# Kernel tuning notes

Measured on AMD Instinct MI355X. Metric: run time of the kernel, lower is better.

The kernel has to match this reference:

```python
import jax, jax.numpy as jnp
import numpy as np

V, T, E, H, B, S = 50000, 45, 256, 512, 32, 256


def setup_inputs() -> dict:
    key = jax.random.key(0)
    ks = jax.random.split(key, 14)
    s = 0.05
    return dict(
        x=jax.random.randint(ks[0], (B, S), 0, V),
        tags=jax.random.randint(ks[1], (B, S), 0, T),
        mask=jnp.ones((B, S), dtype=bool),
        emb=jax.random.normal(ks[2], (V, E), jnp.float32),
        Wih_f=jax.random.normal(ks[3], (4 * H, E), jnp.float32) * s,
        Whh_f=jax.random.normal(ks[4], (4 * H, H), jnp.float32) * s,
        bih_f=jnp.zeros((4 * H,), jnp.float32),
        bhh_f=jnp.zeros((4 * H,), jnp.float32),
        Wih_b=jax.random.normal(ks[5], (4 * H, E), jnp.float32) * s,
        Whh_b=jax.random.normal(ks[6], (4 * H, H), jnp.float32) * s,
        bih_b=jnp.zeros((4 * H,), jnp.float32),
        bhh_b=jnp.zeros((4 * H,), jnp.float32),
        Wout=jax.random.normal(ks[7], (T, 2 * H), jnp.float32) * s,
        bout=jnp.zeros((T,), jnp.float32),
        start=jax.random.normal(ks[8], (T,), jnp.float32) * 0.1,
        end=jax.random.normal(ks[9], (T,), jnp.float32) * 0.1,
        trans=jax.random.normal(ks[10], (T, T), jnp.float32) * 0.1,
    )


def _lstm_dir(xp, Whh, reverse):
    # xp: [S, B, 4H] precomputed input projection + biases; gate order i,f,g,o (torch)
    Bn = xp.shape[1]
    Hn = Whh.shape[1]
    def step(carry, g_in):
        h, c = carry
        g = g_in + h @ Whh.T
        i, f, gg, o = jnp.split(g, 4, axis=-1)
        c = jax.nn.sigmoid(f) * c + jax.nn.sigmoid(i) * jnp.tanh(gg)
        h = jax.nn.sigmoid(o) * jnp.tanh(c)
        return (h, c), h
    init = (jnp.zeros((Bn, Hn), xp.dtype), jnp.zeros((Bn, Hn), xp.dtype))
    _, hs = jax.lax.scan(step, init, xp, reverse=reverse)
    return hs  # [S, B, H]


def _crf_nll(emissions, tags, mask, start, end, trans):
    # emissions: [B, S, T]; neg mean log-likelihood (torchcrf, reduction='mean')
    mf = mask.astype(emissions.dtype)
    em_tag = jnp.take_along_axis(emissions, tags[:, :, None], axis=2)[:, :, 0]  # [B,S]
    num = start[tags[:, 0]] + em_tag[:, 0]
    num = num + ((trans[tags[:, :-1], tags[:, 1:]] + em_tag[:, 1:]) * mf[:, 1:]).sum(1)
    seq_ends = mf.sum(1).astype(tags.dtype) - 1
    last_tags = jnp.take_along_axis(tags, seq_ends[:, None], axis=1)[:, 0]
    num = num + end[last_tags]
    def denom_step(alpha, inp):
        em_t, m_t = inp  # [B,T], [B]
        nxt = jax.nn.logsumexp(alpha[:, :, None] + trans[None, :, :] + em_t[:, None, :], axis=1)
        return jnp.where(m_t[:, None] > 0, nxt, alpha), None
    alpha0 = start[None, :] + emissions[:, 0]
    em_rest = emissions.transpose(1, 0, 2)[1:]  # [S-1, B, T]
    alpha, _ = jax.lax.scan(denom_step, alpha0, (em_rest, mf.T[1:]))
    logZ = jax.nn.logsumexp(alpha + end[None, :], axis=1)
    return -(num - logZ).mean()


def reference(x, tags, mask, emb, Wih_f, Whh_f, bih_f, bhh_f,
              Wih_b, Whh_b, bih_b, bhh_b, Wout, bout, start, end, trans):
    embeds = emb[x]                      # [B, S, E]
    xs = embeds.transpose(1, 0, 2)       # [S, B, E]
    xp_f = jnp.einsum('sbe,ge->sbg', xs, Wih_f) + bih_f + bhh_f
    hs_f = _lstm_dir(xp_f, Whh_f, False)
    xp_b = jnp.einsum('sbe,ge->sbg', xs, Wih_b) + bih_b + bhh_b
    hs_b = _lstm_dir(xp_b, Whh_b, True)
    hcat = jnp.concatenate([hs_f, hs_b], axis=-1)          # [S, B, 2H]
    emissions = jnp.einsum('sbh,th->sbt', hcat, Wout) + bout
    emissions = emissions.transpose(1, 0, 2)                # [B, S, T]
    return _crf_nll(emissions, tags, mask, start, end, trans)
```

## Files before the change

kernel.cpp:

```cpp
#include <hip/hip_runtime.h>
#include <stdint.h>

#define S_LEN 256
#define B_N 32
#define H_N 512
#define E_N 256
#define T_N 45
#define G4H 2048

typedef unsigned short u16;
typedef unsigned int u32;
typedef u16 u16x8 __attribute__((ext_vector_type(8)));
typedef u16 u16x4 __attribute__((ext_vector_type(4)));
typedef u32 u32x4 __attribute__((ext_vector_type(4)));
typedef __bf16 bf16x8 __attribute__((ext_vector_type(8)));
typedef float f32x4 __attribute__((ext_vector_type(4)));
typedef unsigned long long u64;

#define OFF_FLG   0ull
#define OFF_ATOK  1024ull
#define OFF_WIHF  (OFF_ATOK + 4194304ull)
#define OFF_WIHB  (OFF_WIHF + 1048576ull)
#define OFF_WHHF  (OFF_WIHB + 1048576ull)
#define OFF_WHHB  (OFF_WHHF + 2097152ull)
#define OFF_WOUT  (OFF_WHHB + 2097152ull)
#define OFF_BSF   (OFF_WOUT + 98304ull)
#define OFF_BSB   (OFF_BSF + 8192ull)
#define OFF_XPF   (OFF_BSB + 8192ull)
#define OFF_XPB   (OFF_XPF + 33554432ull)
#define OFF_HSF   (OFF_XPB + 33554432ull)
#define OFF_HSB   (OFF_HSF + 8421376ull)
#define OFF_EM    (OFF_HSB + 8421376ull)
#define OFF_VAL   (OFF_EM + 1572864ull)

__device__ __forceinline__ u16 f2bf(float f) {
  union { float f; unsigned u; } v; v.f = f;
  unsigned r = v.u + 0x7FFFu + ((v.u >> 16) & 1u);
  return (u16)(r >> 16);
}
__device__ __forceinline__ float bf2f(u16 b) {
  union { unsigned u; float f; } v; v.u = ((unsigned)b) << 16;
  return v.f;
}
__device__ __forceinline__ bf16x8 ld8(const u16* p) {
  u16x8 v = *reinterpret_cast<const u16x8*>(p);
  return __builtin_bit_cast(bf16x8, v);
}
__device__ __forceinline__ void st_h8cc(u16* p, u16x4 v) {
  __hip_atomic_store(reinterpret_cast<u64*>(p), __builtin_bit_cast(u64, v),
                     __ATOMIC_RELAXED, __HIP_MEMORY_SCOPE_AGENT);
}
__device__ __forceinline__ u32x4 ld16cc(const u16* p) {
  u32x4 r;
  asm volatile("global_load_dwordx4 %0, %1, off sc0 sc1"
               : "=v"(r) : "v"(p) : "memory");
  return r;
}
__device__ __forceinline__ f32x4 mfma16(bf16x8 a, bf16x8 b, f32x4 c) {
  return __builtin_amdgcn_mfma_f32_16x16x32_bf16(a, b, c, 0, 0, 0);
}
__device__ __forceinline__ float sigm(float x) { return 1.f / (1.f + __expf(-x)); }
__device__ __forceinline__ float tanhf_(float x) {
  float ax = fabsf(x);
  float e = __expf(-2.f * ax);
  float t = 1.f - 2.f * e / (1.f + e);
  return (x < 0.f) ? -t : t;
}
__device__ __forceinline__ float wredmax(float v) {
  #pragma unroll
  for (int m = 1; m < 64; m <<= 1) v = fmaxf(v, __shfl_xor(v, m));
  return v;
}
__device__ __forceinline__ float wredsum(float v) {
  #pragma unroll
  for (int m = 1; m < 64; m <<= 1) v += __shfl_xor(v, m);
  return v;
}

__global__ void k_castA(const int* __restrict__ x, const float* __restrict__ emb,
                        u16* __restrict__ atok) {
  int idx = blockIdx.x * 256 + threadIdx.x;
  int t = idx >> 5;
  int e0 = (idx & 31) << 3;
  int s = t >> 5, b = t & 31;
  int xid = x[b * S_LEN + s];
  const float4* p = reinterpret_cast<const float4*>(emb + (size_t)xid * E_N + e0);
  float4 lo = p[0], hi = p[1];
  u16x8 o;
  o[0] = f2bf(lo.x); o[1] = f2bf(lo.y); o[2] = f2bf(lo.z); o[3] = f2bf(lo.w);
  o[4] = f2bf(hi.x); o[5] = f2bf(hi.y); o[6] = f2bf(hi.z); o[7] = f2bf(hi.w);
  *reinterpret_cast<u16x8*>(atok + (size_t)t * E_N + e0) = o;
}

__global__ void k_castW(const float* __restrict__ WihF, const float* __restrict__ WihB,
                        const float* __restrict__ WhhF, const float* __restrict__ WhhB,
                        const float* __restrict__ Wout,
                        const float* __restrict__ bihF, const float* __restrict__ bhhF,
                        const float* __restrict__ bihB, const float* __restrict__ bhhB,
                        u16* wihf, u16* wihb, u16* whhf, u16* whhb, u16* woutp,
                        float* bsf, float* bsb, u16* hsf, u16* hsb) {
  int i = blockIdx.x * 256 + threadIdx.x;
  if (i < 524288) { wihf[i] = f2bf(WihF[i]); return; }
  i -= 524288;
  if (i < 524288) { wihb[i] = f2bf(WihB[i]); return; }
  i -= 524288;
  if (i < 1048576) { whhf[i] = f2bf(WhhF[i]); return; }
  i -= 1048576;
  if (i < 1048576) { whhb[i] = f2bf(WhhB[i]); return; }
  i -= 1048576;
  if (i < 49152) {
    int n = i >> 10, k = i & 1023;
    woutp[i] = (n < T_N) ? f2bf(Wout[n * 1024 + k]) : (u16)0;
    return;
  }
  i -= 49152;
  if (i < 2048) { bsf[i] = bihF[i] + bhhF[i]; return; }
  i -= 2048;
  if (i < 2048) { bsb[i] = bihB[i] + bhhB[i]; return; }
  i -= 2048;
  if (i < 16384) { hsf[i] = 0; return; }
  i -= 16384;
  if (i < 16384) { hsb[(size_t)256 * 16384 + i] = 0; return; }
}

__global__ __launch_bounds__(256) void k_gemm_xp(
    const u16* __restrict__ atok, const u16* __restrict__ wihF, const u16* __restrict__ wihB,
    const float* __restrict__ bsF, const float* __restrict__ bsB,
    u16* __restrict__ xpF, u16* __restrict__ xpB) {
  int wid = blockIdx.x;
  int dir = wid >> 10, rem = wid & 1023;
  const int wave = threadIdx.x >> 6, lane = threadIdx.x & 63;
  const int lr = lane & 15, lh = lane >> 4;
  const int t0 = (rem >> 3) * 64;
  const int g0 = (rem & 7) * 256 + wave * 64;
  const u16* wih = dir ? wihB : wihF;
  const float* bs = dir ? bsB : bsF;
  u16* xp = dir ? xpB : xpF;
  f32x4 acc[4][4] = {};
  for (int kk = 0; kk < 8; ++kk) {
    int e = kk * 32 + lh * 8;
    bf16x8 a[4], bfr[4];
    #pragma unroll
    for (int mi = 0; mi < 4; ++mi) a[mi] = ld8(atok + (size_t)(t0 + 16 * mi + lr) * E_N + e);
    #pragma unroll
    for (int ni = 0; ni < 4; ++ni) bfr[ni] = ld8(wih + (size_t)(g0 + 16 * ni + lr) * E_N + e);
    #pragma unroll
    for (int mi = 0; mi < 4; ++mi)
      #pragma unroll
      for (int ni = 0; ni < 4; ++ni) acc[mi][ni] = mfma16(a[mi], bfr[ni], acc[mi][ni]);
  }
  #pragma unroll
  for (int ni = 0; ni < 4; ++ni) {
    int g = g0 + 16 * ni + lr;
    float bsv = bs[g];
    #pragma unroll
    for (int mi = 0; mi < 4; ++mi)
      #pragma unroll
      for (int r = 0; r < 4; ++r) {
        int t = t0 + 16 * mi + 4 * lh + r;
        xp[(size_t)t * G4H + g] = f2bf(acc[mi][ni][r] + bsv);
      }
  }
}

__global__ __launch_bounds__(128, 1) void k_lstm(
    const u16* __restrict__ whhF, const u16* __restrict__ whhB,
    const u16* __restrict__ xpF, const u16* __restrict__ xpB,
    u16* __restrict__ hsF, u16* __restrict__ hsB, int* flags) {
  const int dir = blockIdx.x >> 5;
  const int w = blockIdx.x & 31;
  const int nt = threadIdx.x >> 6;
  const int lane = threadIdx.x & 63;
  const int lr = lane & 15, lh = lane >> 4;
  const u16* whh = dir ? whhB : whhF;
  const u16* xp = dir ? xpB : xpF;
  u16* hs = dir ? hsB : hsF;
  int* flg = flags + dir * 64;
  const int myf = w * 2 + nt;

  bf16x8 A[4][16];
  #pragma unroll
  for (int mt = 0; mt < 4; ++mt) {
    const u16* base = whh + (size_t)(mt * 512 + 16 * w + lr) * H_N + lh * 8;
    #pragma unroll
    for (int kk = 0; kk < 16; ++kk) A[mt][kk] = ld8(base + kk * 32);
  }
  const int b = nt * 16 + lr;
  const int j0 = 16 * w + 4 * lh;
  float cst[4] = {0.f, 0.f, 0.f, 0.f};

  for (int t = 0; t < S_LEN; ++t) {
    const int s = dir ? (S_LEN - 1 - t) : t;
    const int slot_r = dir ? (s + 1) : s;
    const int slot_w = dir ? s : (s + 1);
    u16x4 xq[4];
    const u16* xpt = xp + ((size_t)(s * B_N + b)) * G4H + j0;
    #pragma unroll
    for (int mt = 0; mt < 4; ++mt) xq[mt] = *reinterpret_cast<const u16x4*>(xpt + mt * 512);

    if (t > 0) {
      for (;;) {
        int f = __hip_atomic_load(&flg[lane], __ATOMIC_RELAXED, __HIP_MEMORY_SCOPE_AGENT);
        if (__all(f >= t)) break;
        __builtin_amdgcn_s_sleep(1);
      }
    }

    const u16* hp = hs + ((size_t)slot_r * B_N + b) * H_N + lh * 8;
    u32x4 raw[16];
    #pragma unroll
    for (int kk = 0; kk < 16; ++kk) raw[kk] = ld16cc(hp + kk * 32);
    asm volatile("s_waitcnt vmcnt(0)" ::: "memory");
    __builtin_amdgcn_sched_barrier(0);

    f32x4 acc[4] = {};
    #pragma unroll
    for (int kk = 0; kk < 16; ++kk) {
      bf16x8 Bf = __builtin_bit_cast(bf16x8, raw[kk]);
      #pragma unroll
      for (int mt = 0; mt < 4; ++mt) acc[mt] = mfma16(A[mt][kk], Bf, acc[mt]);
    }
    u16x4 hv;
    #pragma unroll
    for (int r = 0; r < 4; ++r) {
      float gi = acc[0][r] + bf2f(xq[0][r]);
      float gf = acc[1][r] + bf2f(xq[1][r]);
      float gg = acc[2][r] + bf2f(xq[2][r]);
      float go = acc[3][r] + bf2f(xq[3][r]);
      float c = sigm(gf) * cst[r] + sigm(gi) * tanhf_(gg);
      cst[r] = c;
      hv[r] = f2bf(sigm(go) * tanhf_(c));
    }
    st_h8cc(hs + ((size_t)slot_w * B_N + b) * H_N + j0, hv);
    asm volatile("s_waitcnt vmcnt(0)" ::: "memory");
    if (lane == 0)
      __hip_atomic_store(&flg[myf], t + 1, __ATOMIC_RELAXED, __HIP_MEMORY_SCOPE_AGENT);
  }
}

__global__ __launch_bounds__(256) void k_gemm_em(
    const u16* __restrict__ hsF, const u16* __restrict__ hsB,
    const u16* __restrict__ woutp, const float* __restrict__ bout, float* __restrict__ em) {
  const int wave = threadIdx.x >> 6, lane = threadIdx.x & 63;
  const int lr = lane & 15, lh = lane >> 4;
  const int t0 = blockIdx.x * 64 + wave * 16;
  f32x4 acc[3] = {};
  for (int kk = 0; kk < 32; ++kk) {
    int k = kk * 32 + lh * 8;
    int t = t0 + lr;
    int s = t >> 5, bt = t & 31;
    const u16* ap = (kk < 16) ? (hsF + ((size_t)(s + 1) * B_N + bt) * H_N + k)
                              : (hsB + ((size_t)s * B_N + bt) * H_N + (k - 512));
    bf16x8 a = ld8(ap);
    #pragma unroll
    for (int ni = 0; ni < 3; ++ni) {
      bf16x8 bb = ld8(woutp + (size_t)(16 * ni + lr) * 1024 + k);
      acc[ni] = mfma16(a, bb, acc[ni]);
    }
  }
  #pragma unroll
  for (int ni = 0; ni < 3; ++ni) {
    int tag = 16 * ni + lr;
    float bo = (tag < T_N) ? bout[tag] : 0.f;
    #pragma unroll
    for (int r = 0; r < 4; ++r) {
      int t = t0 + 4 * lh + r;
      em[(size_t)t * 48 + tag] = acc[ni][r] + bo;
    }
  }
}

__global__ __launch_bounds__(64) void k_crf(
    const float* __restrict__ em, const int* __restrict__ tags,
    const float* __restrict__ start, const float* __restrict__ endv,
    const float* __restrict__ trans, float* __restrict__ val) {
  __shared__ float tl[T_N * T_N + 32];
  const int b = blockIdx.x;
  const int lane = threadIdx.x;
  for (int i = lane; i < T_N * T_N + 32; i += 64)
    tl[i] = (i < T_N * T_N) ? trans[i] : 0.f;
  __syncthreads();
  float acur = (lane < T_N) ? (start[lane] + em[(size_t)b * 48 + lane]) : -1e30f;
  for (int s = 1; s < S_LEN; ++s) {
    float shift = wredmax(acur);
    float emv = (lane < 48) ? em[((size_t)s * B_N + b) * 48 + lane] : 0.f;
    float s0 = 0.f, s1 = 0.f, s2 = 0.f;
    #pragma unroll
    for (int t = 0; t < T_N; t += 3) {
      s0 += __expf(__shfl(acur, t)     + tl[t * T_N + lane]       - shift);
      s1 += __expf(__shfl(acur, t + 1) + tl[(t + 1) * T_N + lane] - shift);
      s2 += __expf(__shfl(acur, t + 2) + tl[(t + 2) * T_N + lane] - shift);
    }
    acur = (lane < T_N) ? (shift + __logf(s0 + s1 + s2) + emv) : -1e30f;
  }
  float z = (lane < T_N) ? (acur + endv[lane]) : -1e30f;
  float m = wredmax(z);
  float sum = wredsum((lane < T_N) ? __expf(z - m) : 0.f);
  float logZ = m + __logf(sum);
  float np = 0.f;
  #pragma unroll
  for (int q = 0; q < 4; ++q) {
    int s = 1 + lane * 4 + q;
    if (s < S_LEN) {
      int tp = tags[b * S_LEN + s - 1], tc = tags[b * S_LEN + s];
      np += tl[tp * T_N + tc] + em[((size_t)s * B_N + b) * 48 + tc];
    }
  }
  np = wredsum(np);
  if (lane == 0) {
    int tg0 = tags[b * S_LEN], tgL = tags[b * S_LEN + S_LEN - 1];
    float num = start[tg0] + em[(size_t)b * 48 + tg0] + np + endv[tgL];
    val[b] = num - logZ;
  }
}

__global__ void k_final(const float* __restrict__ val, float* __restrict__ out) {
  int lane = threadIdx.x & 63;
  float v = (lane < B_N) ? val[lane] : 0.f;
  v = wredsum(v);
  if (threadIdx.x == 0) out[0] = -(v / (float)B_N);
}

extern "C" void kernel_launch(void* const* d_in, const int* in_sizes, int n_in,
                              void* d_out, int out_size, void* d_ws, size_t ws_size,
                              hipStream_t stream) {
  const int* x = (const int*)d_in[0];
  const int* tags = (const int*)d_in[1];
  const float* emb = (const float*)d_in[3];
  const float* WihF = (const float*)d_in[4];
  const float* WhhF = (const float*)d_in[5];
  const float* bihF = (const float*)d_in[6];
  const float* bhhF = (const float*)d_in[7];
  const float* WihB = (const float*)d_in[8];
  const float* WhhB = (const float*)d_in[9];
  const float* bihB = (const float*)d_in[10];
  const float* bhhB = (const float*)d_in[11];
  const float* Wout = (const float*)d_in[12];
  const float* bout = (const float*)d_in[13];
  const float* start = (const float*)d_in[14];
  const float* endv = (const float*)d_in[15];
  const float* trans = (const float*)d_in[16];
  float* out = (float*)d_out;
  char* ws = (char*)d_ws;

  u16* atok = (u16*)(ws + OFF_ATOK);
  u16* wihf = (u16*)(ws + OFF_WIHF);
  u16* wihb = (u16*)(ws + OFF_WIHB);
  u16* whhf = (u16*)(ws + OFF_WHHF);
  u16* whhb = (u16*)(ws + OFF_WHHB);
  u16* woutp = (u16*)(ws + OFF_WOUT);
  float* bsf = (float*)(ws + OFF_BSF);
  float* bsb = (float*)(ws + OFF_BSB);
  u16* xpf = (u16*)(ws + OFF_XPF);
  u16* xpb = (u16*)(ws + OFF_XPB);
  u16* hsf = (u16*)(ws + OFF_HSF);
  u16* hsb = (u16*)(ws + OFF_HSB);
  float* emis = (float*)(ws + OFF_EM);
  float* val = (float*)(ws + OFF_VAL);

  hipMemsetAsync(ws + OFF_FLG, 0, 1024, stream);
  k_castA<<<1024, 256, 0, stream>>>(x, emb, atok);
  k_castW<<<12624, 256, 0, stream>>>(WihF, WihB, WhhF, WhhB, Wout, bihF, bhhF, bihB, bhhB,
                                     wihf, wihb, whhf, whhb, woutp, bsf, bsb, hsf, hsb);
  k_gemm_xp<<<2048, 256, 0, stream>>>(atok, wihf, wihb, bsf, bsb, xpf, xpb);
  k_lstm<<<64, 128, 0, stream>>>(whhf, whhb, xpf, xpb, hsf, hsb, (int*)(ws + OFF_FLG));
  k_gemm_em<<<128, 256, 0, stream>>>(hsf, hsb, woutp, bout, emis);
  k_crf<<<32, 64, 0, stream>>>(emis, tags, start, endv, trans, val);
  k_final<<<1, 64, 0, stream>>>(val, out);
}
```

Measured before the change: 1.740 ms.

## Replace LSTM flag-based step sync with sentinel-valued hidden state polling

Removes the per-step atomic flag spin-wait and flag store in the persistent LSTM kernel. The hidden-state buffers are prefilled with 0xFF sentinels, and each wave re-polls only those h chunks that still hold the sentinel, so data arrival itself signals readiness. This cuts one round-trip of flag store, wait and load per timestep. It relies on a bf16 pair never legitimately encoding as 0xFFFFFFFF (a NaN pattern) and on 16-byte stores being seen atomically. It also adds two 8 MB memsets before the kernels.

```diff
diff --git a/kernel.cpp b/kernel.cpp
--- a/kernel.cpp
+++ b/kernel.cpp
@@ -17,8 +17,7 @@
 typedef float f32x4 __attribute__((ext_vector_type(4)));
 typedef unsigned long long u64;
 
-#define OFF_FLG   0ull
-#define OFF_ATOK  1024ull
+#define OFF_ATOK  256ull
 #define OFF_WIHF  (OFF_ATOK + 4194304ull)
 #define OFF_WIHB  (OFF_WIHF + 1048576ull)
 #define OFF_WHHF  (OFF_WIHB + 1048576ull)
@@ -166,7 +165,7 @@
 __global__ __launch_bounds__(128, 1) void k_lstm(
     const u16* __restrict__ whhF, const u16* __restrict__ whhB,
     const u16* __restrict__ xpF, const u16* __restrict__ xpB,
-    u16* __restrict__ hsF, u16* __restrict__ hsB, int* flags) {
+    u16* __restrict__ hsF, u16* __restrict__ hsB) {
   const int dir = blockIdx.x >> 5;
   const int w = blockIdx.x & 31;
   const int nt = threadIdx.x >> 6;
@@ -175,8 +174,6 @@
   const u16* whh = dir ? whhB : whhF;
   const u16* xp = dir ? xpB : xpF;
   u16* hs = dir ? hsB : hsF;
-  int* flg = flags + dir * 64;
-  const int myf = w * 2 + nt;
 
   bf16x8 A[4][16];
   #pragma unroll
@@ -198,20 +195,29 @@
     #pragma unroll
     for (int mt = 0; mt < 4; ++mt) xq[mt] = *reinterpret_cast<const u16x4*>(xpt + mt * 512);
 
-    if (t > 0) {
-      for (;;) {
-        int f = __hip_atomic_load(&flg[lane], __ATOMIC_RELAXED, __HIP_MEMORY_SCOPE_AGENT);
-        if (__all(f >= t)) break;
-        __builtin_amdgcn_s_sleep(1);
-      }
-    }
-
     const u16* hp = hs + ((size_t)slot_r * B_N + b) * H_N + lh * 8;
     u32x4 raw[16];
     #pragma unroll
     for (int kk = 0; kk < 16; ++kk) raw[kk] = ld16cc(hp + kk * 32);
     asm volatile("s_waitcnt vmcnt(0)" ::: "memory");
     __builtin_amdgcn_sched_barrier(0);
+    u32 pend = 0;
+    #pragma unroll
+    for (int kk = 0; kk < 16; ++kk)
+      if (raw[kk][0] == 0xFFFFFFFFu || raw[kk][2] == 0xFFFFFFFFu) pend |= (1u << kk);
+    while (__builtin_amdgcn_ballot_w64(pend != 0u)) {
+      #pragma unroll
+      for (int kk = 0; kk < 16; ++kk)
+        if (pend & (1u << kk)) raw[kk] = ld16cc(hp + kk * 32);
+      asm volatile("s_waitcnt vmcnt(0)" ::: "memory");
+      __builtin_amdgcn_sched_barrier(0);
+      u32 np = 0;
+      #pragma unroll
+      for (int kk = 0; kk < 16; ++kk)
+        if ((pend & (1u << kk)) &&
+            (raw[kk][0] == 0xFFFFFFFFu || raw[kk][2] == 0xFFFFFFFFu)) np |= (1u << kk);
+      pend = np;
+    }
 
     f32x4 acc[4] = {};
     #pragma unroll
@@ -232,9 +238,6 @@
       hv[r] = f2bf(sigm(go) * tanhf_(c));
     }
     st_h8cc(hs + ((size_t)slot_w * B_N + b) * H_N + j0, hv);
-    asm volatile("s_waitcnt vmcnt(0)" ::: "memory");
-    if (lane == 0)
-      __hip_atomic_store(&flg[myf], t + 1, __ATOMIC_RELAXED, __HIP_MEMORY_SCOPE_AGENT);
   }
 }
 
@@ -358,12 +361,13 @@
   float* emis = (float*)(ws + OFF_EM);
   float* val = (float*)(ws + OFF_VAL);
 
-  hipMemsetAsync(ws + OFF_FLG, 0, 1024, stream);
+  hipMemsetAsync(ws + OFF_HSF + 32768ull, 0xFF, 8388608ull, stream);
+  hipMemsetAsync(ws + OFF_HSB, 0xFF, 8388608ull, stream);
   k_castA<<<1024, 256, 0, stream>>>(x, emb, atok);
   k_castW<<<12624, 256, 0, stream>>>(WihF, WihB, WhhF, WhhB, Wout, bihF, bhhF, bihB, bhhB,
                                      wihf, wihb, whhf, whhb, woutp, bsf, bsb, hsf, hsb);
   k_gemm_xp<<<2048, 256, 0, stream>>>(atok, wihf, wihb, bsf, bsb, xpf, xpb);
-  k_lstm<<<64, 128, 0, stream>>>(whhf, whhb, xpf, xpb, hsf, hsb, (int*)(ws + OFF_FLG));
+  k_lstm<<<64, 128, 0, stream>>>(whhf, whhb, xpf, xpb, hsf, hsb);
   k_gemm_em<<<128, 256, 0, stream>>>(hsf, hsb, woutp, bout, emis);
   k_crf<<<32, 64, 0, stream>>>(emis, tags, start, endv, trans, val);
   k_final<<<1, 64, 0, stream>>>(val, out);
```

Result: faster. 1.530 ms (-12.1%).
